# Optimization experiments

Hardware: AMD Instinct MI355X
Metric: run time of the kernel (lower is better)

Reference implementation:

```python
import jax, jax.numpy as jnp
import numpy as np

# Geometry / model constants
WD, WH, WW = 2, 7, 7          # window size
SD, SH, SW = 1, 3, 3          # shift size
DIM, NH = 96, 3               # channels per half, heads
HD = DIM // NH                # head dim = 32
MLP = 4 * DIM
B, D, H, W = 2, 16, 56, 56    # D,H,W divisible by window -> no padding
N = WD * WH * WW              # tokens per window = 98
NWIN = (D // WD) * (H // WH) * (W // WW)  # 512


def window_partition(x):
    # x: [b, d, h, w, c] -> [b*nW, N, c]  (works for np and jnp arrays)
    b, d, h, w, c = x.shape
    x = x.reshape(b, d // WD, WD, h // WH, WH, w // WW, WW, c)
    return x.transpose(0, 1, 3, 5, 2, 4, 6, 7).reshape(-1, N, c)


def window_reverse(win, b, d, h, w):
    # [b*nW, N, c] -> [b, d, h, w, c]
    c = win.shape[-1]
    x = win.reshape(b, d // WD, h // WH, w // WW, WD, WH, WW, c)
    return x.transpose(0, 1, 4, 2, 5, 3, 6, 7).reshape(b, d, h, w, c)


def _rel_index():
    coords = np.stack(np.meshgrid(np.arange(WD), np.arange(WH), np.arange(WW), indexing='ij'))
    coords = coords.reshape(3, -1)                      # [3, N]
    rel = (coords[:, :, None] - coords[:, None, :]).transpose(1, 2, 0)  # [N, N, 3]
    rel[:, :, 0] += WD - 1; rel[:, :, 1] += WH - 1; rel[:, :, 2] += WW - 1
    rel[:, :, 0] *= (2 * WH - 1) * (2 * WW - 1)
    rel[:, :, 1] *= (2 * WW - 1)
    return rel.sum(-1).astype(np.int32)                 # [N, N]


def _compute_mask():
    img = np.zeros((1, D, H, W, 1), np.float32)
    cnt = 0
    for d in (slice(0, -WD), slice(-WD, -SD), slice(-SD, None)):
        for h in (slice(0, -WH), slice(-WH, -SH), slice(-SH, None)):
            for w in (slice(0, -WW), slice(-WW, -SW), slice(-SW, None)):
                img[:, d, h, w, :] = cnt; cnt += 1
    mw = window_partition(img).squeeze(-1)              # [nW, N]
    diff = mw[:, None, :] - mw[:, :, None]
    return np.where(diff != 0, np.float32(-100.0), np.float32(0.0))


def layernorm(x, g, b, eps=1e-5):
    m = x.mean(-1, keepdims=True)
    v = ((x - m) ** 2).mean(-1, keepdims=True)
    return (x - m) * jax.lax.rsqrt(v + eps) * g + b


def setup_inputs() -> dict:
    key = jax.random.key(0)
    ks = jax.random.split(key, 8)
    s = 0.02
    return {
        'x': jax.random.normal(ks[0], (B, D, H, W, 2 * DIM), jnp.float32),
        'mask_matrix': jnp.asarray(_compute_mask()),
        'rel_index': jnp.asarray(_rel_index()),
        'norm1_g': jnp.ones((DIM,), jnp.float32), 'norm1_b': jnp.zeros((DIM,), jnp.float32),
        'qkv_w': s * jax.random.normal(ks[1], (3 * DIM, DIM), jnp.float32),
        'qkv_b': jnp.zeros((3 * DIM,), jnp.float32),
        'rel_bias_table': s * jax.random.normal(ks[2], ((2 * WD - 1) * (2 * WH - 1) * (2 * WW - 1), NH), jnp.float32),
        'proj_w': s * jax.random.normal(ks[3], (DIM, DIM), jnp.float32),
        'proj_b': jnp.zeros((DIM,), jnp.float32),
        'norm2_g': jnp.ones((DIM,), jnp.float32), 'norm2_b': jnp.zeros((DIM,), jnp.float32),
        'fc1_w': s * jax.random.normal(ks[4], (MLP, DIM), jnp.float32),
        'fc1_b': jnp.zeros((MLP,), jnp.float32),
        'fc2_w': s * jax.random.normal(ks[5], (DIM, MLP), jnp.float32),
        'fc2_b': jnp.zeros((DIM,), jnp.float32),
    }


def reference(x, mask_matrix, rel_index, norm1_g, norm1_b, qkv_w, qkv_b,
              rel_bias_table, proj_w, proj_b, norm2_g, norm2_b,
              fc1_w, fc1_b, fc2_w, fc2_b):
    x1, x2 = jnp.split(x, 2, axis=-1)                   # each [B,D,H,W,DIM]

    # ---- F branch: shifted windowed attention on x2 ----
    xn = layernorm(x2, norm1_g, norm1_b)
    shifted = jnp.roll(xn, (-SD, -SH, -SW), axis=(1, 2, 3))
    xw = window_partition(shifted)                      # [B*nW, N, DIM]
    qkv = (xw @ qkv_w.T + qkv_b).reshape(-1, N, 3, NH, HD).transpose(2, 0, 3, 1, 4)
    q, k, v = qkv[0], qkv[1], qkv[2]                    # [B*nW, NH, N, HD]
    attn = jnp.einsum('bhnd,bhmd->bhnm', q, k) * (HD ** -0.5)
    bias = rel_bias_table[rel_index.reshape(-1)].reshape(N, N, NH).transpose(2, 0, 1)
    attn = attn + bias[None]
    attn = attn.reshape(B, NWIN, NH, N, N) + mask_matrix[None, :, None]
    attn = jax.nn.softmax(attn.reshape(-1, NH, N, N), axis=-1)
    out = jnp.einsum('bhnm,bhmd->bhnd', attn, v).transpose(0, 2, 1, 3).reshape(-1, N, DIM)
    out = out @ proj_w.T + proj_b
    out = window_reverse(out, B, D, H, W)
    out = jnp.roll(out, (SD, SH, SW), axis=(1, 2, 3))
    y1 = x1 + out

    # ---- G branch: MLP on y1 ----
    g = layernorm(y1, norm2_g, norm2_b)
    g = jax.nn.gelu(g @ fc1_w.T + fc1_b, approximate=False) @ fc2_w.T + fc2_b
    y2 = x2 + g

    return jnp.concatenate([y1, y2], axis=-1)
```

## Files before the change

kernel.cpp:

```cpp
#include <hip/hip_runtime.h>
#include <math.h>

typedef unsigned int u32;
typedef unsigned short u16;

typedef __attribute__((ext_vector_type(8))) short bf16x8;
typedef __attribute__((ext_vector_type(4))) float f32x4;

#define NTOK 98
#define NWIN 1024

#define XS_STR 104
#define QK_STR 40
#define P_STR  136
#define Q_BASE 13328
#define K_BASE 17808
#define VT_BASE 22288
#define LDS_U16 26640

#define COMB_U16 344064

__device__ __forceinline__ float bflo(u32 u){ union{u32 i; float f;} c; c.i = u<<16; return c.f; }
__device__ __forceinline__ float bfhi(u32 u){ union{u32 i; float f;} c; c.i = u & 0xffff0000u; return c.f; }
__device__ __forceinline__ u16 f2bf(float f){
  union{float f; u32 i;} c; c.f = f;
  u32 x = c.i;
  return (u16)((x + 0x7fffu + ((x>>16)&1u)) >> 16);
}

__device__ __forceinline__ float gelu_f(float v){
  float t = __expf(-1.702f * v);
  return v * __builtin_amdgcn_rcpf(1.f + t);
}

__device__ __forceinline__ int src_token(int win, int t){
  int b  = win >> 9;
  int wr = win & 511;
  int db = wr >> 6, hb = (wr >> 3) & 7, wb = wr & 7;
  int di = t / 49, r = t - di*49;
  int hi = r / 7,  wi = r - hi*7;
  int d = (db*2 + di + 1) & 15;
  int h = hb*7 + hi + 3; if (h >= 56) h -= 56;
  int w = wb*7 + wi + 3; if (w >= 56) w -= 56;
  return ((b*16 + d)*56 + h)*56 + w;
}

__global__ __launch_bounds__(256) void k0_prep(const float* __restrict__ qkvw,
    const float* __restrict__ qkvb, const float* __restrict__ pw,
    const float* __restrict__ w1, const float* __restrict__ w2,
    u16* __restrict__ Wb, float* __restrict__ bs){
  int i = blockIdx.x*256 + threadIdx.x;
  if (i < 288*96){
    float v = qkvw[i];
    if (i < 96*96) v *= 0.17677669529663687f;
    Wb[i] = f2bf(v);
  } else if (i < 288*96 + 96*96){
    Wb[i] = f2bf(pw[i - 288*96]);
  } else if (i < 288*96 + 96*96 + 384*96){
    Wb[i] = f2bf(w1[i - (288*96 + 96*96)]);
  } else if (i < 288*96 + 96*96 + 384*96 + 96*384){
    Wb[i] = f2bf(w2[i - (288*96 + 96*96 + 384*96)]);
  }
  if (i < 288){
    float v = qkvb[i];
    if (i < 96) v *= 0.17677669529663687f;
    bs[i] = v;
  }
}

__global__ __launch_bounds__(256) void k0b_comb(const float* __restrict__ bias_tab,
    const int* __restrict__ rel_idx, const float* __restrict__ mask,
    u16* __restrict__ comb){
  int idx = blockIdx.x*256 + threadIdx.x;
  if (idx >= COMB_U16) return;
  int m   = idx / 43008;  int r1 = idx - m*43008;
  int hd  = r1 / 14336;   int r2 = r1 - hd*14336;
  int mt  = r2 / 2048;    int r3 = r2 - mt*2048;
  int rr  = r3 / 512;     int r4 = r3 - rr*512;
  int ntp = r4 / 128;     int r5 = r4 - ntp*128;
  int ln  = r5 >> 1;      int half = r5 & 1;
  int lg  = ln >> 4,      l15 = ln & 15;
  int nt  = ntp*2 + half;
  int i   = mt*16 + lg*4 + rr;
  int j   = nt*16 + l15;
  float v = -1e30f;
  if (i < 98 && j < 98){
    int wr = ((m>>2)&1)*448 + ((m>>1)&1)*56 + (m&1)*7;
    v = bias_tab[rel_idx[i*98+j]*3 + hd] + mask[(size_t)wr*9604 + i*98 + j];
  }
  comb[idx] = f2bf(v);
}

__global__ __launch_bounds__(256) void k1_ln(const float* __restrict__ x,
      const float* __restrict__ g, const float* __restrict__ bb, u16* __restrict__ xn){
  int wid  = (blockIdx.x << 2) + (threadIdx.x >> 6);
  int lane = threadIdx.x & 63;
  if (wid >= NWIN*NTOK) return;
  int win = wid / NTOK, t = wid - win*NTOK;
  int tok = src_token(win, t);
  const float* xp = x + (size_t)tok*192 + 96;
  float a0 = 0.f, a1 = 0.f;
  if (lane < 48){ float2 v = *(const float2*)(xp + (lane<<1)); a0 = v.x; a1 = v.y; }
  float s = a0 + a1, s2 = a0*a0 + a1*a1;
  #pragma unroll
  for (int o = 32; o; o >>= 1){ s += __shfl_xor(s, o); s2 += __shfl_xor(s2, o); }
  float mean = s * (1.f/96.f);
  float rstd = rsqrtf(s2*(1.f/96.f) - mean*mean + 1e-5f);
  if (lane < 48){
    float r0 = (a0-mean)*rstd*g[2*lane]   + bb[2*lane];
    float r1 = (a1-mean)*rstd*g[2*lane+1] + bb[2*lane+1];
    u32 pk = (u32)f2bf(r0) | ((u32)f2bf(r1) << 16);
    *(u32*)(xn + (size_t)wid*96 + (lane<<1)) = pk;
  }
}

__global__ __launch_bounds__(256) void k2_attn(const u16* __restrict__ xn,
    const u16* __restrict__ Wb, const float* __restrict__ bs,
    const u16* __restrict__ comb, u16* __restrict__ attn_o){
  __shared__ __align__(16) u16 lds[LDS_U16];
  int tid  = threadIdx.x;
  int lane = tid & 63, wv = tid >> 6;
  int l15  = lane & 15, lg = lane >> 4;
  int j = blockIdx.x;
  int group = j / 24, r24 = j - group*24;
  int win = group*8 + (r24 & 7);
  int hd  = r24 >> 3;

  {
    const u32* xw = (const u32*)(xn + (size_t)win*98*96);
    u32* xs32 = (u32*)lds;
    for (int i = tid; i < 98*48; i += 256){
      int r = i/48, c = i - r*48;
      xs32[r*52 + c] = xw[i];
    }
    for (int i = tid; i < 14*52; i += 256){
      int r = 98 + i/52, c = i - (i/52)*52;
      xs32[r*52 + c] = 0;
    }
    u32* vt32 = (u32*)(lds + VT_BASE);
    for (int i = tid; i < 32*12; i += 256){
      int d = i/12, c = i - d*12;
      vt32[d*68 + 56 + c] = 0;
    }
  }
  __syncthreads();

  for (int t = wv; t < 42; t += 4){
    f32x4 acc = {0.f,0.f,0.f,0.f};
    if (t < 28){
      int tt = (t < 14) ? t : t - 14;
      int mt = tt >> 1, nt = tt & 1;
      int ch = hd*32 + nt*16 + l15 + ((t < 14) ? 0 : 96);
      const u16* wrow = Wb + ch*96 + lg*8;
      const u16* xsrow = lds + (mt*16 + l15)*XS_STR;
      #pragma unroll
      for (int ks = 0; ks < 3; ks++){
        bf16x8 a = *(const bf16x8*)(xsrow + ks*32 + lg*8);
        bf16x8 b = *(const bf16x8*)(wrow + ks*32);
        acc = __builtin_amdgcn_mfma_f32_16x16x32_bf16(a, b, acc, 0, 0, 0);
      }
      float bias = bs[ch];
      u16* dst = lds + ((t < 14) ? Q_BASE : K_BASE);
      int col = nt*16 + l15;
      int rbase = mt*16 + lg*4;
      #pragma unroll
      for (int r = 0; r < 4; r++)
        dst[(rbase+r)*QK_STR + col] = f2bf(acc[r] + bias);
    } else {
      int tt = t - 28; int mt = tt/7, nt = tt - mt*7;
      int ch = 192 + hd*32 + mt*16 + l15;
      const u16* wrow = Wb + ch*96 + lg*8;
      const u16* xsrow = lds + (nt*16 + l15)*XS_STR;
      #pragma unroll
      for (int ks = 0; ks < 3; ks++){
        bf16x8 a = *(const bf16x8*)(wrow + ks*32);
        bf16x8 b = *(const bf16x8*)(xsrow + ks*32 + lg*8);
        acc = __builtin_amdgcn_mfma_f32_16x16x32_bf16(a, b, acc, 0, 0, 0);
      }
      int dbase = mt*16 + lg*4;
      #pragma unroll
      for (int r = 0; r < 4; r++){
        float bias = bs[192 + hd*32 + dbase + r];
        lds[VT_BASE + (dbase+r)*P_STR + nt*16 + l15] = f2bf(acc[r] + bias);
      }
    }
  }
  __syncthreads();

  {
    int wr = win & 511;
    int maskid = ((wr>>6)==7)*4 + (((wr>>3)&7)==7)*2 + ((wr&7)==7);
    const u32* cb_base = (const u32*)comb + (size_t)(maskid*3 + hd)*7168 + lane;

    for (int mt = wv; mt < 7; mt += 4){
      {
        u32* p32 = (u32*)lds;
        int rmax = (mt == 6) ? 2 : 16;
        for (int i = lane; i < rmax*12; i += 64){
          int rr = i/12, c = i - rr*12;
          p32[(mt*16+rr)*68 + 56 + c] = 0;
        }
      }
      int ibase = mt*16 + lg*4;
      const u32* cbm = cb_base + mt*1024;
      float cb[4][7];
      #pragma unroll
      for (int r = 0; r < 4; r++){
        #pragma unroll
        for (int ntp = 0; ntp < 4; ntp++){
          u32 pk = cbm[(r*4 + ntp)*64];
          cb[r][2*ntp] = bflo(pk);
          if (2*ntp + 1 < 7) cb[r][2*ntp+1] = bfhi(pk);
        }
      }
      const u16* qrow = lds + Q_BASE + (mt*16 + l15)*QK_STR;
      bf16x8 a = *(const bf16x8*)(qrow + lg*8);
      f32x4 s[7];
      #pragma unroll
      for (int nt = 0; nt < 7; nt++){
        const u16* krow = lds + K_BASE + (nt*16 + l15)*QK_STR;
        bf16x8 b = *(const bf16x8*)(krow + lg*8);
        f32x4 z = {0.f,0.f,0.f,0.f};
        s[nt] = __builtin_amdgcn_mfma_f32_16x16x32_bf16(a, b, z, 0, 0, 0);
      }
      #pragma unroll
      for (int r = 0; r < 4; r++){
        int i = ibase + r;
        float sv[7];
        float mx = -3.0e38f;
        #pragma unroll
        for (int nt = 0; nt < 7; nt++){
          float v = s[nt][r] + cb[r][nt];
          sv[nt] = v; mx = fmaxf(mx, v);
        }
        #pragma unroll
        for (int off = 1; off < 16; off <<= 1) mx = fmaxf(mx, __shfl_xor(mx, off));
        float sum = 0.f;
        #pragma unroll
        for (int nt = 0; nt < 7; nt++){
          float e = __expf(sv[nt] - mx);
          sv[nt] = e; sum += e;
        }
        #pragma unroll
        for (int off = 1; off < 16; off <<= 1) sum += __shfl_xor(sum, off);
        float inv = 1.f / sum;
        if (i < 98){
          #pragma unroll
          for (int nt = 0; nt < 7; nt++)
            lds[i*P_STR + nt*16 + l15] = f2bf(sv[nt]*inv);
        }
      }
    }
  }
  __syncthreads();

  for (int t = wv; t < 14; t += 4){
    int mt = t >> 1, nt = t & 1;
    const u16* prow = lds + (mt*16 + l15)*P_STR;
    const u16* vrow = lds + VT_BASE + (nt*16 + l15)*P_STR;
    f32x4 acc = {0.f,0.f,0.f,0.f};
    #pragma unroll
    for (int ks = 0; ks < 4; ks++){
      bf16x8 a = *(const bf16x8*)(prow + ks*32 + lg*8);
      bf16x8 b = *(const bf16x8*)(vrow + ks*32 + lg*8);
      acc = __builtin_amdgcn_mfma_f32_16x16x32_bf16(a, b, acc, 0, 0, 0);
    }
    int ibase = mt*16 + lg*4;
    int d = nt*16 + l15;
    #pragma unroll
    for (int r = 0; r < 4; r++){
      int i = ibase + r;
      if (i < 98) attn_o[((size_t)win*98 + i)*96 + hd*32 + d] = f2bf(acc[r]);
    }
  }
}

#define HS 392
#define X1F_U16 3328
#define YN_U16 12544
#define WT_U16 15872
__global__ __launch_bounds__(256, 5) void k34_projmlp(const u16* __restrict__ attn_o,
    const u16* __restrict__ Pwb, const float* __restrict__ pb,
    const float* __restrict__ g2, const float* __restrict__ b2,
    const u16* __restrict__ W1b, const float* __restrict__ b1,
    const u16* __restrict__ W2b, const float* __restrict__ bb2,
    const float* __restrict__ x, float* __restrict__ out){
  __shared__ __align__(16) u16 lds[15936];
  int tid = threadIdx.x;
  int lane = tid & 63, wv = tid >> 6;
  int l15 = lane & 15, lg = lane >> 4;
  size_t base = (size_t)blockIdx.x * 32;
  float* x1f = (float*)(lds + X1F_U16);
  float* resf = (float*)lds;
  int* wt_s = (int*)(lds + WT_U16);
  int mt = wv & 1, ng = wv >> 1;

  if (tid < 32){
    int tok = (int)base + tid;
    int b = tok / 50176; int r0 = tok - b*50176;
    int d = r0 / 3136;   int r1 = r0 - d*3136;
    int h = r1 / 56;     int w = r1 - h*56;
    int dd = (d + 15) & 15;
    int db = dd >> 1, di = dd & 1;
    int hh = h - 3; if (hh < 0) hh += 56;
    int hb = hh / 7, hi = hh - hb*7;
    int ww = w - 3; if (ww < 0) ww += 56;
    int wb = ww / 7, wi = ww - wb*7;
    wt_s[tid] = (b*512 + db*64 + hb*8 + wb)*98 + di*49 + hi*7 + wi;
  }
  __syncthreads();

  {
    const u32* src = (const u32*)attn_o;
    u32* aw32 = (u32*)lds;
    #pragma unroll
    for (int k = 0; k < 6; k++){
      int i = tid + k*256;
      int r = i/48, c = i - r*48;
      aw32[r*52 + c] = src[(size_t)wt_s[r]*48 + c];
    }
    #pragma unroll
    for (int k = 0; k < 3; k++){
      int i = tid + k*256;
      int tk = i/24, c4 = i - tk*24;
      float4 v = *(const float4*)(x + (base + tk)*192 + c4*4);
      *(float4*)(x1f + tk*100 + c4*4) = v;
    }
  }
  __syncthreads();

  {
    const u16* a0p = lds + l15*104 + lg*8;
    const u16* a1p = a0p + 16*104;
    bf16x8 a00=*(const bf16x8*)(a0p), a01=*(const bf16x8*)(a0p+32), a02=*(const bf16x8*)(a0p+64);
    bf16x8 a10=*(const bf16x8*)(a1p), a11=*(const bf16x8*)(a1p+32), a12=*(const bf16x8*)(a1p+64);
    for (int nt = wv; nt < 6; nt += 4){
      const u16* wrow = Pwb + (nt*16 + l15)*96 + lg*8;
      bf16x8 w0=*(const bf16x8*)(wrow), w1=*(const bf16x8*)(wrow+32), w2=*(const bf16x8*)(wrow+64);
      f32x4 acc0 = {0.f,0.f,0.f,0.f}, acc1 = {0.f,0.f,0.f,0.f};
      acc0 = __builtin_amdgcn_mfma_f32_16x16x32_bf16(a00, w0, acc0, 0, 0, 0);
      acc1 = __builtin_amdgcn_mfma_f32_16x16x32_bf16(a10, w0, acc1, 0, 0, 0);
      acc0 = __builtin_amdgcn_mfma_f32_16x16x32_bf16(a01, w1, acc0, 0, 0, 0);
      acc1 = __builtin_amdgcn_mfma_f32_16x16x32_bf16(a11, w1, acc1, 0, 0, 0);
      acc0 = __builtin_amdgcn_mfma_f32_16x16x32_bf16(a02, w2, acc0, 0, 0, 0);
      acc1 = __builtin_amdgcn_mfma_f32_16x16x32_bf16(a12, w2, acc1, 0, 0, 0);
      int n = nt*16 + l15;
      float bias = pb[n];
      #pragma unroll
      for (int r = 0; r < 4; r++){
        int row = lg*4 + r;
        x1f[row*100 + n] = acc0[r] + bias + x1f[row*100 + n];
      }
      #pragma unroll
      for (int r = 0; r < 4; r++){
        int row = 16 + lg*4 + r;
        x1f[row*100 + n] = acc1[r] + bias + x1f[row*100 + n];
      }
    }
  }
  __syncthreads();

  {
    #pragma unroll
    for (int k = 0; k < 3; k++){
      int i = tid + k*256;
      int tk = i/24, c4 = i - tk*24;
      *(float4*)(out + (base + tk)*192 + c4*4) = *(const float4*)(x1f + tk*100 + c4*4);
    }
    int tk = tid >> 3, c8 = tid & 7;
    const float4* yp = (const float4*)(x1f + tk*100 + c8*12);
    float4 v4[3];
    #pragma unroll
    for (int j = 0; j < 3; j++) v4[j] = yp[j];
    float s = 0.f, s2 = 0.f;
    #pragma unroll
    for (int j = 0; j < 3; j++){
      s  += v4[j].x + v4[j].y + v4[j].z + v4[j].w;
      s2 += v4[j].x*v4[j].x + v4[j].y*v4[j].y + v4[j].z*v4[j].z + v4[j].w*v4[j].w;
    }
    s  += __shfl_xor(s, 1);  s  += __shfl_xor(s, 2);  s  += __shfl_xor(s, 4);
    s2 += __shfl_xor(s2, 1); s2 += __shfl_xor(s2, 2); s2 += __shfl_xor(s2, 4);
    float mean = s * (1.f/96.f);
    float rstd = rsqrtf(s2*(1.f/96.f) - mean*mean + 1e-5f);
    u32* dst = (u32*)(lds + YN_U16) + tk*52 + c8*6;
    const float* gp = g2 + c8*12;
    const float* bp = b2 + c8*12;
    #pragma unroll
    for (int p = 0; p < 6; p++){
      float e0 = (p & 1) ? v4[p>>1].z : v4[p>>1].x;
      float e1 = (p & 1) ? v4[p>>1].w : v4[p>>1].y;
      float r0 = (e0 - mean)*rstd*gp[2*p]   + bp[2*p];
      float r1 = (e1 - mean)*rstd*gp[2*p+1] + bp[2*p+1];
      dst[p] = (u32)f2bf(r0) | ((u32)f2bf(r1) << 16);
    }
  }
  __syncthreads();

  {
    const u16* a0p = lds + YN_U16 + l15*104 + lg*8;
    const u16* a1p = a0p + 16*104;
    bf16x8 a00=*(const bf16x8*)(a0p), a01=*(const bf16x8*)(a0p+32), a02=*(const bf16x8*)(a0p+64);
    bf16x8 a10=*(const bf16x8*)(a1p), a11=*(const bf16x8*)(a1p+32), a12=*(const bf16x8*)(a1p+64);
    #pragma unroll
    for (int q = 0; q < 6; q++){
      const u16* wrow = W1b + ((wv*6 + q)*16 + l15)*96 + lg*8;
      bf16x8 w0=*(const bf16x8*)(wrow), w1=*(const bf16x8*)(wrow+32), w2=*(const bf16x8*)(wrow+64);
      f32x4 acc0 = {0.f,0.f,0.f,0.f}, acc1 = {0.f,0.f,0.f,0.f};
      acc0 = __builtin_amdgcn_mfma_f32_16x16x32_bf16(a00, w0, acc0, 0, 0, 0);
      acc1 = __builtin_amdgcn_mfma_f32_16x16x32_bf16(a10, w0, acc1, 0, 0, 0);
      acc0 = __builtin_amdgcn_mfma_f32_16x16x32_bf16(a01, w1, acc0, 0, 0, 0);
      acc1 = __builtin_amdgcn_mfma_f32_16x16x32_bf16(a11, w1, acc1, 0, 0, 0);
      acc0 = __builtin_amdgcn_mfma_f32_16x16x32_bf16(a02, w2, acc0, 0, 0, 0);
      acc1 = __builtin_amdgcn_mfma_f32_16x16x32_bf16(a12, w2, acc1, 0, 0, 0);
      int n = (wv*6 + q)*16 + l15;
      float bias = b1[n];
      #pragma unroll
      for (int r = 0; r < 4; r++)
        lds[(lg*4 + r)*HS + n] = f2bf(gelu_f(acc0[r] + bias));
      #pragma unroll
      for (int r = 0; r < 4; r++)
        lds[(16 + lg*4 + r)*HS + n] = f2bf(gelu_f(acc1[r] + bias));
    }
  }
  __syncthreads();

  f32x4 res0, res1, res2;
  {
    const u16* arow = lds + (mt*16 + l15)*HS + lg*8;
    const u16* w2p = W2b + ((ng*3)*16 + l15)*384 + lg*8;
    #pragma unroll
    for (int q = 0; q < 3; q++){
      f32x4 aA = {0.f,0.f,0.f,0.f}, aB = {0.f,0.f,0.f,0.f};
      #pragma unroll
      for (int ks = 0; ks < 6; ks++){
        bf16x8 x0 = *(const bf16x8*)(arow + ks*32);
        bf16x8 x1 = *(const bf16x8*)(arow + (ks+6)*32);
        bf16x8 wa = *(const bf16x8*)(w2p + q*6144 + ks*32);
        bf16x8 wb = *(const bf16x8*)(w2p + q*6144 + (ks+6)*32);
        aA = __builtin_amdgcn_mfma_f32_16x16x32_bf16(x0, wa, aA, 0, 0, 0);
        aB = __builtin_amdgcn_mfma_f32_16x16x32_bf16(x1, wb, aB, 0, 0, 0);
      }
      f32x4 rr;
      #pragma unroll
      for (int r = 0; r < 4; r++) rr[r] = aA[r] + aB[r];
      if (q == 0) res0 = rr; else if (q == 1) res1 = rr; else res2 = rr;
    }
  }
  __syncthreads();

  {
    int c0 = (ng*3)*16 + l15;
    float b0 = bb2[c0], b1v = bb2[c0+16], b2v = bb2[c0+32];
    #pragma unroll
    for (int r = 0; r < 4; r++){
      int row = mt*16 + lg*4 + r;
      resf[row*100 + c0]      = res0[r] + b0;
      resf[row*100 + c0 + 16] = res1[r] + b1v;
      resf[row*100 + c0 + 32] = res2[r] + b2v;
    }
  }
  __syncthreads();

  {
    #pragma unroll
    for (int k = 0; k < 3; k++){
      int i = tid + k*256;
      int tk = i/24, c4 = i - tk*24;
      float4 a = *(const float4*)(resf + tk*100 + c4*4);
      float4 b = *(const float4*)(x + (base + tk)*192 + 96 + c4*4);
      float4 o; o.x = a.x + b.x; o.y = a.y + b.y; o.z = a.z + b.z; o.w = a.w + b.w;
      *(float4*)(out + (base + tk)*192 + 96 + c4*4) = o;
    }
  }
}

extern "C" void kernel_launch(void* const* d_in, const int* in_sizes, int n_in,
                              void* d_out, int out_size, void* d_ws, size_t ws_size,
                              hipStream_t stream){
  const float* x    = (const float*)d_in[0];
  const float* mask = (const float*)d_in[1];
  const int*   reli = (const int*)d_in[2];
  const float* n1g  = (const float*)d_in[3];
  const float* n1b  = (const float*)d_in[4];
  const float* qkvw = (const float*)d_in[5];
  const float* qkvb = (const float*)d_in[6];
  const float* btab = (const float*)d_in[7];
  const float* pw   = (const float*)d_in[8];
  const float* pb   = (const float*)d_in[9];
  const float* n2g  = (const float*)d_in[10];
  const float* n2b  = (const float*)d_in[11];
  const float* w1   = (const float*)d_in[12];
  const float* b1   = (const float*)d_in[13];
  const float* w2   = (const float*)d_in[14];
  const float* b2   = (const float*)d_in[15];
  float* out = (float*)d_out;

  u16* xn   = (u16*)d_ws;
  u16* attn = xn + (size_t)NWIN*98*96;
  u16* Wb   = attn + (size_t)NWIN*98*96;
  u16* Pwb  = Wb + 288*96;
  u16* W1b  = Pwb + 96*96;
  u16* W2b  = W1b + 384*96;
  float* bsc = (float*)(W2b + 96*384);
  u16* comb = (u16*)(bsc + 288);

  k0_prep<<<432,   256, 0, stream>>>(qkvw, qkvb, pw, w1, w2, Wb, bsc);
  k0b_comb<<<1344, 256, 0, stream>>>(btab, reli, mask, comb);
  k1_ln  <<<25088, 256, 0, stream>>>(x, n1g, n1b, xn);
  k2_attn<<<3072,  256, 0, stream>>>(xn, Wb, bsc, comb, attn);
  k34_projmlp<<<3136, 256, 0, stream>>>(attn, Pwb, pb, n2g, n2b,
                                        W1b, b1, W2b, b2, x, out);
}
```

Measured before the change: 175.0 us.

## Stage MLP weights through LDS in chunks and split FC2 over K halves

The FC1 and FC2 weights are now copied cooperatively into a shared LDS staging buffer in six chunks, instead of each wave loading its weight fragments directly from global memory. FC2 is restructured so the two wave pairs each handle half of the 384-wide K dimension across all output columns, and the partial sums are combined in LDS with a two-phase write and add. This aims to coalesce weight reads and spread FC2 work evenly across waves. In exchange it adds about a dozen extra barriers, more LDS use, and lowers the occupancy hint from 5 to 4 blocks.

```diff
diff --git a/kernel.cpp b/kernel.cpp
--- a/kernel.cpp
+++ b/kernel.cpp
@@ -278,22 +278,24 @@
 #define HS 392
 #define X1F_U16 3328
 #define YN_U16 12544
-#define WT_U16 15872
-__global__ __launch_bounds__(256, 5) void k34_projmlp(const u16* __restrict__ attn_o,
+#define S_U16 12544
+#define WT_U16 18816
+__global__ __launch_bounds__(256, 4) void k34_projmlp(const u16* __restrict__ attn_o,
     const u16* __restrict__ Pwb, const float* __restrict__ pb,
     const float* __restrict__ g2, const float* __restrict__ b2,
     const u16* __restrict__ W1b, const float* __restrict__ b1,
     const u16* __restrict__ W2b, const float* __restrict__ bb2,
     const float* __restrict__ x, float* __restrict__ out){
-  __shared__ __align__(16) u16 lds[15936];
+  __shared__ __align__(16) u16 lds[18880];
   int tid = threadIdx.x;
   int lane = tid & 63, wv = tid >> 6;
   int l15 = lane & 15, lg = lane >> 4;
   size_t base = (size_t)blockIdx.x * 32;
   float* x1f = (float*)(lds + X1F_U16);
   float* resf = (float*)lds;
+  u16* S = lds + S_U16;
   int* wt_s = (int*)(lds + WT_U16);
-  int mt = wv & 1, ng = wv >> 1;
+  int mt = wv & 1, kh = wv >> 1;
 
   if (tid < 32){
     int tok = (int)base + tid;
@@ -396,14 +398,25 @@
   }
   __syncthreads();
 
+  bf16x8 a00, a01, a02, a10, a11, a12;
   {
     const u16* a0p = lds + YN_U16 + l15*104 + lg*8;
     const u16* a1p = a0p + 16*104;
-    bf16x8 a00=*(const bf16x8*)(a0p), a01=*(const bf16x8*)(a0p+32), a02=*(const bf16x8*)(a0p+64);
-    bf16x8 a10=*(const bf16x8*)(a1p), a11=*(const bf16x8*)(a1p+32), a12=*(const bf16x8*)(a1p+64);
-    #pragma unroll
-    for (int q = 0; q < 6; q++){
-      const u16* wrow = W1b + ((wv*6 + q)*16 + l15)*96 + lg*8;
+    a00 = *(const bf16x8*)(a0p); a01 = *(const bf16x8*)(a0p+32); a02 = *(const bf16x8*)(a0p+64);
+    a10 = *(const bf16x8*)(a1p); a11 = *(const bf16x8*)(a1p+32); a12 = *(const bf16x8*)(a1p+64);
+  }
+  __syncthreads();
+
+  for (int c = 0; c < 6; c++){
+    {
+      const u32* srcw = (const u32*)(W1b + c*64*96);
+      u32* dstw = (u32*)S;
+      #pragma unroll
+      for (int k = 0; k < 12; k++) dstw[tid + k*256] = srcw[tid + k*256];
+    }
+    __syncthreads();
+    {
+      const u16* wrow = S + (wv*16 + l15)*96 + lg*8;
       bf16x8 w0=*(const bf16x8*)(wrow), w1=*(const bf16x8*)(wrow+32), w2=*(const bf16x8*)(wrow+64);
       f32x4 acc0 = {0.f,0.f,0.f,0.f}, acc1 = {0.f,0.f,0.f,0.f};
       acc0 = __builtin_amdgcn_mfma_f32_16x16x32_bf16(a00, w0, acc0, 0, 0, 0);
@@ -412,7 +425,7 @@
       acc1 = __builtin_amdgcn_mfma_f32_16x16x32_bf16(a11, w1, acc1, 0, 0, 0);
       acc0 = __builtin_amdgcn_mfma_f32_16x16x32_bf16(a02, w2, acc0, 0, 0, 0);
       acc1 = __builtin_amdgcn_mfma_f32_16x16x32_bf16(a12, w2, acc1, 0, 0, 0);
-      int n = (wv*6 + q)*16 + l15;
+      int n = (c*4 + wv)*16 + l15;
       float bias = b1[n];
       #pragma unroll
       for (int r = 0; r < 4; r++)
@@ -421,42 +434,60 @@
       for (int r = 0; r < 4; r++)
         lds[(16 + lg*4 + r)*HS + n] = f2bf(gelu_f(acc1[r] + bias));
     }
-  }
-  __syncthreads();
-
-  f32x4 res0, res1, res2;
-  {
-    const u16* arow = lds + (mt*16 + l15)*HS + lg*8;
-    const u16* w2p = W2b + ((ng*3)*16 + l15)*384 + lg*8;
-    #pragma unroll
-    for (int q = 0; q < 3; q++){
-      f32x4 aA = {0.f,0.f,0.f,0.f}, aB = {0.f,0.f,0.f,0.f};
+    __syncthreads();
+  }
+
+  f32x4 res0, res1, res2, res3, res4, res5;
+  #pragma unroll
+  for (int c = 0; c < 6; c++){
+    {
+      const u32* srcw = (const u32*)(W2b + c*16*384);
+      u32* dstw = (u32*)S;
+      #pragma unroll
+      for (int k = 0; k < 12; k++){
+        int i = tid + k*256;
+        int row = i / 192, col = i - row*192;
+        dstw[row*196 + col] = srcw[i];
+      }
+    }
+    __syncthreads();
+    {
+      const u16* arow = lds + (mt*16 + l15)*HS + kh*192 + lg*8;
+      const u16* wrow = S + l15*392 + kh*192 + lg*8;
+      f32x4 acc = {0.f,0.f,0.f,0.f};
       #pragma unroll
       for (int ks = 0; ks < 6; ks++){
-        bf16x8 x0 = *(const bf16x8*)(arow + ks*32);
-        bf16x8 x1 = *(const bf16x8*)(arow + (ks+6)*32);
-        bf16x8 wa = *(const bf16x8*)(w2p + q*6144 + ks*32);
-        bf16x8 wb = *(const bf16x8*)(w2p + q*6144 + (ks+6)*32);
-        aA = __builtin_amdgcn_mfma_f32_16x16x32_bf16(x0, wa, aA, 0, 0, 0);
-        aB = __builtin_amdgcn_mfma_f32_16x16x32_bf16(x1, wb, aB, 0, 0, 0);
-      }
-      f32x4 rr;
-      #pragma unroll
-      for (int r = 0; r < 4; r++) rr[r] = aA[r] + aB[r];
-      if (q == 0) res0 = rr; else if (q == 1) res1 = rr; else res2 = rr;
-    }
-  }
-  __syncthreads();
-
-  {
-    int c0 = (ng*3)*16 + l15;
-    float b0 = bb2[c0], b1v = bb2[c0+16], b2v = bb2[c0+32];
-    #pragma unroll
-    for (int r = 0; r < 4; r++){
-      int row = mt*16 + lg*4 + r;
-      resf[row*100 + c0]      = res0[r] + b0;
-      resf[row*100 + c0 + 16] = res1[r] + b1v;
-      resf[row*100 + c0 + 32] = res2[r] + b2v;
+        bf16x8 xa = *(const bf16x8*)(arow + ks*32);
+        bf16x8 wa = *(const bf16x8*)(wrow + ks*32);
+        acc = __builtin_amdgcn_mfma_f32_16x16x32_bf16(xa, wa, acc, 0, 0, 0);
+      }
+      if (c == 0) res0 = acc; else if (c == 1) res1 = acc;
+      else if (c == 2) res2 = acc; else if (c == 3) res3 = acc;
+      else if (c == 4) res4 = acc; else res5 = acc;
+    }
+    __syncthreads();
+  }
+
+  if (kh == 0){
+    #pragma unroll
+    for (int c = 0; c < 6; c++){
+      f32x4 rc = (c==0)?res0:(c==1)?res1:(c==2)?res2:(c==3)?res3:(c==4)?res4:res5;
+      int col = c*16 + l15;
+      float bias = bb2[col];
+      #pragma unroll
+      for (int r = 0; r < 4; r++)
+        resf[(mt*16 + lg*4 + r)*100 + col] = rc[r] + bias;
+    }
+  }
+  __syncthreads();
+  if (kh == 1){
+    #pragma unroll
+    for (int c = 0; c < 6; c++){
+      f32x4 rc = (c==0)?res0:(c==1)?res1:(c==2)?res2:(c==3)?res3:(c==4)?res4:res5;
+      int col = c*16 + l15;
+      #pragma unroll
+      for (int r = 0; r < 4; r++)
+        resf[(mt*16 + lg*4 + r)*100 + col] += rc[r];
     }
   }
   __syncthreads();
```

Measured after the change: 161.7 us. 7.6% less time.
